# Kernel optimization log

Measured on AMD Instinct MI355X. Metric: run time of the kernel, lower is better.

The kernel has to match this reference:

```python
import jax, jax.numpy as jnp
import numpy as np

B, S, H = 2, 2048, 4096
NH, NKV, D = 32, 8, 128  # heads, kv heads, head_dim


def rotate_half(x):
    x1, x2 = jnp.split(x, 2, axis=-1)
    return jnp.concatenate((-x2, x1), axis=-1)


def setup_inputs() -> dict:
    key = jax.random.key(0)
    ks = jax.random.split(key, 5)
    hidden_states = jax.random.normal(ks[0], (B, S, H), jnp.float32) * 0.02
    wq = jax.random.normal(ks[1], (H, NH * D), jnp.float32) * 0.02
    wk = jax.random.normal(ks[2], (H, NKV * D), jnp.float32) * 0.02
    wv = jax.random.normal(ks[3], (H, NKV * D), jnp.float32) * 0.02
    wo = jax.random.normal(ks[4], (NH * D, H), jnp.float32) * 0.02
    # Llama rotary cache: emb = cat(freqs, freqs); cos/sin shape [S, D]
    inv_freq = 1.0 / (10000.0 ** (jnp.arange(0, D, 2, dtype=jnp.float32) / D))
    t = jnp.arange(S, dtype=jnp.float32)
    freqs = jnp.einsum('i,j->ij', t, inv_freq)
    emb = jnp.concatenate((freqs, freqs), axis=-1)
    cos, sin = jnp.cos(emb), jnp.sin(emb)
    # additive causal mask [S, S]
    causal = jnp.tril(jnp.ones((S, S), dtype=bool))
    attn_mask = jnp.where(causal, 0.0, -1e9).astype(jnp.float32)
    return {'hidden_states': hidden_states, 'wq': wq, 'wk': wk, 'wv': wv,
            'wo': wo, 'cos': cos, 'sin': sin, 'attn_mask': attn_mask}


def reference(hidden_states, wq, wk, wv, wo, cos, sin, attn_mask):
    b, s, _ = hidden_states.shape
    q = (hidden_states @ wq).reshape(b, s, NH, D)   # [b,s,nh,d]
    k = (hidden_states @ wk).reshape(b, s, NKV, D)  # [b,s,nkv,d]
    v = (hidden_states @ wv).reshape(b, s, NKV, D)
    c = cos[None, :, None, :]  # [1,s,1,d]
    sn = sin[None, :, None, :]
    q = q * c + rotate_half(q) * sn
    k = k * c + rotate_half(k) * sn
    # GQA: repeat KV heads to match query heads
    grp = NH // NKV
    k = jnp.repeat(k, grp, axis=2)
    v = jnp.repeat(v, grp, axis=2)
    scale = 1.0 / np.sqrt(D).astype(np.float32)
    scores = jnp.einsum('bqhd,bkhd->bhqk', q, k) * scale
    scores = scores + attn_mask[None, None, :, :]
    probs = jax.nn.softmax(scores, axis=-1)
    out = jnp.einsum('bhqk,bkhd->bqhd', probs, v).reshape(b, s, NH * D)
    return out @ wo
```

## Files before the change

### kernel.cpp

```cpp
#include <hip/hip_runtime.h>

typedef __attribute__((ext_vector_type(8))) short short8;
typedef __attribute__((ext_vector_type(4))) float f32x4;
typedef __attribute__((ext_vector_type(4))) int int4v;

__device__ __forceinline__ float bf2f(unsigned short u) {
  unsigned int x = ((unsigned int)u) << 16;
  float f;
  __builtin_memcpy(&f, &x, 4);
  return f;
}
__device__ __forceinline__ unsigned short f2bf(float f) {
  unsigned int x;
  __builtin_memcpy(&x, &f, 4);
  unsigned int r = (x + 0x7FFFu + ((x >> 16) & 1u)) >> 16;
  return (unsigned short)r;
}
__device__ __forceinline__ unsigned int cvtpk_bf16(float lo, float hi) {
  unsigned int r;
  asm("v_cvt_pk_bf16_f32 %0, %1, %2" : "=v"(r) : "v"(lo), "v"(hi));
  return r;
}
__device__ __forceinline__ float exp2_hw(float x) {
  float r;
  asm("v_exp_f32 %0, %1" : "=v"(r) : "v"(x));
  return r;
}
__device__ __forceinline__ int4v s8_to_i4(short8 v) {
  int4v r;
  __builtin_memcpy(&r, &v, 16);
  return r;
}
__device__ __forceinline__ short8 i4_to_s8(int4v v) {
  short8 r;
  __builtin_memcpy(&r, &v, 16);
  return r;
}
__device__ __forceinline__ short8 ld8_f32(const float* p) {
  f32x4 x = *(const f32x4*)p;
  f32x4 y = *(const f32x4*)(p + 4);
  short8 r;
  r[0] = (short)f2bf(x[0]); r[1] = (short)f2bf(x[1]);
  r[2] = (short)f2bf(x[2]); r[3] = (short)f2bf(x[3]);
  r[4] = (short)f2bf(y[0]); r[5] = (short)f2bf(y[1]);
  r[6] = (short)f2bf(y[2]); r[7] = (short)f2bf(y[3]);
  return r;
}

__device__ __forceinline__ void async16(unsigned short* lds, const unsigned short* g) {
  __builtin_amdgcn_global_load_lds(
      (const __attribute__((address_space(1))) void*)g,
      (__attribute__((address_space(3))) void*)lds, 16, 0, 0);
}

__global__ void downcast_f2b(const float* __restrict__ in,
                             unsigned short* __restrict__ out, int n8) {
  int i = blockIdx.x * 256 + threadIdx.x;
  if (i >= n8) return;
  *(short8*)(out + (size_t)i * 8) = ld8_f32(in + (size_t)i * 8);
}

__global__ void transpose64_f2b(const float* __restrict__ in,
                                unsigned short* __restrict__ out, int R, int C) {
  alignas(16) __shared__ unsigned short t[64][72];
  const int c0 = blockIdx.x * 64;
  const int r0 = blockIdx.y * 64;
  const int tid = threadIdx.x;
  const int rr = tid >> 4;
  const int cc = (tid & 15) << 2;
#pragma unroll
  for (int i = 0; i < 4; i++) {
    int r = rr + i * 16;
    f32x4 v = *(const f32x4*)(in + (size_t)(r0 + r) * C + c0 + cc);
#pragma unroll
    for (int j = 0; j < 4; j++) t[cc + j][r] = f2bf(v[j]);
  }
  __syncthreads();
  const int seg = tid & 7;
  const int cr = tid >> 3;
#pragma unroll
  for (int i = 0; i < 2; i++) {
    int c = cr + i * 32;
    short8 w = *(const short8*)&t[c][seg * 8];
    *(short8*)(out + (size_t)(c0 + c) * R + r0 + seg * 8) = w;
  }
}

#define MFMA16(AF, B0, B1, N0, N1)                                                   \
  _Pragma("unroll") for (int mi = 0; mi < 8; mi++) {                                 \
    acc[mi][N0] = __builtin_amdgcn_mfma_f32_16x16x32_bf16(AF[mi], B0, acc[mi][N0], 0, 0, 0); \
    acc[mi][N1] = __builtin_amdgcn_mfma_f32_16x16x32_bf16(AF[mi], B1, acc[mi][N1], 0, 0, 0); \
  }

#define STAGE8(BUF, SLOT, BASE, KOFF)                                     \
  do {                                                                    \
    async16(&lds[BUF][SLOT][tid * 8], (BASE) + (KOFF));                   \
    async16(&lds[BUF][SLOT][4096 + tid * 8], (BASE) + Kstep128 + (KOFF)); \
  } while (0)

#define BAR8 asm volatile("s_barrier" ::: "memory")

#define TILE8(CUR, UU, S0, S123, VM)                                                   \
  do {                                                                                 \
    const int kb = (UU)*64;                                                            \
    short8 af[8], b0, b1;                                                              \
                                                                       \
    _Pragma("unroll") for (int mi = 0; mi < 8; mi++)                                   \
        af[mi] = *(const short8*)(&lds[CUR][0][(wr * 128 + mi * 16 + fr) * 32 + fragoff]); \
    b0 = *(const short8*)(&lds[CUR][2][(wc * 64 + 0 * 16 + fr) * 32 + fragoff]);       \
    b1 = *(const short8*)(&lds[CUR][2][(wc * 64 + 1 * 16 + fr) * 32 + fragoff]);       \
    if (S0) STAGE8((CUR) ^ 1, 3, Bbase, kb + 96);                                      \
    BAR8;                                                                              \
    __builtin_amdgcn_s_setprio(1);                                                     \
    MFMA16(af, b0, b1, 0, 1);                                                          \
    __builtin_amdgcn_s_setprio(0);                                                     \
    BAR8;                                                                              \
                                                                       \
    b0 = *(const short8*)(&lds[CUR][2][(wc * 64 + 2 * 16 + fr) * 32 + fragoff]);       \
    b1 = *(const short8*)(&lds[CUR][2][(wc * 64 + 3 * 16 + fr) * 32 + fragoff]);       \
    if (S123) STAGE8(CUR, 0, Abase, kb + 128);                                         \
    BAR8;                                                                              \
    __builtin_amdgcn_s_setprio(1);                                                     \
    MFMA16(af, b0, b1, 2, 3);                                                          \
    __builtin_amdgcn_s_setprio(0);                                                     \
    BAR8;                                                                              \
                                                                       \
    _Pragma("unroll") for (int mi = 0; mi < 8; mi++)                                   \
        af[mi] = *(const short8*)(&lds[CUR][1][(wr * 128 + mi * 16 + fr) * 32 + fragoff]); \
    b0 = *(const short8*)(&lds[CUR][3][(wc * 64 + 0 * 16 + fr) * 32 + fragoff]);       \
    b1 = *(const short8*)(&lds[CUR][3][(wc * 64 + 1 * 16 + fr) * 32 + fragoff]);       \
    if (S123) STAGE8(CUR, 2, Bbase, kb + 128);                                         \
    BAR8;                                                                              \
    __builtin_amdgcn_s_setprio(1);                                                     \
    MFMA16(af, b0, b1, 0, 1);                                                          \
    __builtin_amdgcn_s_setprio(0);                                                     \
    BAR8;                                                                              \
                                                                       \
    b0 = *(const short8*)(&lds[CUR][3][(wc * 64 + 2 * 16 + fr) * 32 + fragoff]);       \
    b1 = *(const short8*)(&lds[CUR][3][(wc * 64 + 3 * 16 + fr) * 32 + fragoff]);       \
    if (S123) STAGE8(CUR, 1, Abase, kb + 160);                                         \
    BAR8;                                                                              \
    __builtin_amdgcn_s_setprio(1);                                                     \
    MFMA16(af, b0, b1, 2, 3);                                                          \
    __builtin_amdgcn_s_setprio(0);                                                     \
    if ((VM) == 6) {                                                                   \
      asm volatile("s_waitcnt vmcnt(6)" ::: "memory");                                 \
      __builtin_amdgcn_sched_barrier(0);                                               \
    } else if ((VM) == 0) {                                                            \
      asm volatile("s_waitcnt vmcnt(0)" ::: "memory");                                 \
      __builtin_amdgcn_sched_barrier(0);                                               \
    }                                                                                  \
    BAR8;                                                                              \
  } while (0)

template <int CF32>
__global__ __launch_bounds__(512, 2) void gemm8p(
    const unsigned short* __restrict__ A, const unsigned short* __restrict__ BT,
    void* __restrict__ Cp, int M, int N, int K) {
  alignas(16) __shared__ unsigned short lds[2][4][8192];
  const int tid = threadIdx.x;
  const int l = tid & 63;
  const int wv = tid >> 6;
  const int wr = wv >> 2, wc = wv & 3;

  const int nwg = gridDim.x * gridDim.y;
  int id = blockIdx.y * gridDim.x + blockIdx.x;
  id = (id & 7) * (nwg >> 3) + (id >> 3);
  const int bm = (id % gridDim.x) * 256;
  const int bn = (id / gridDim.x) * 256;

  const int fr = l & 15, hi = l >> 4;
  const int fragoff = ((hi ^ (((fr >> 3) & 1) << 1)) << 3);
  const int srow = tid >> 2;
  const int scol = (((tid & 3) ^ (((tid >> 5) & 1) << 1)) << 3);
  const unsigned short* Abase = A + (size_t)(bm + srow) * K + scol;
  const unsigned short* Bbase = BT + (size_t)(bn + srow) * K + scol;
  const size_t Kstep128 = (size_t)128 * K;

  f32x4 acc[8][4] = {};
  const int nt = K >> 6;

  STAGE8(0, 0, Abase, 0);
  STAGE8(0, 2, Bbase, 0);
  STAGE8(0, 1, Abase, 32);
  STAGE8(0, 3, Bbase, 32);
  STAGE8(1, 0, Abase, 64);
  STAGE8(1, 2, Bbase, 64);
  STAGE8(1, 1, Abase, 96);
  asm volatile("s_waitcnt vmcnt(6)" ::: "memory");
  __builtin_amdgcn_sched_barrier(0);
  BAR8;

  int U = 0;
  for (; U + 3 < nt; U += 2) {
    TILE8(0, U, 1, 1, 6);
    TILE8(1, U + 1, 1, 1, 6);
  }
  TILE8(0, nt - 2, 1, 0, 0);
  TILE8(1, nt - 1, 0, 0, -1);

  const int er = hi << 2;
#pragma unroll
  for (int mi = 0; mi < 8; mi++) {
#pragma unroll
    for (int ni = 0; ni < 4; ni++) {
      int row = bm + wr * 128 + mi * 16 + er;
      int col = bn + wc * 64 + ni * 16 + fr;
#pragma unroll
      for (int r = 0; r < 4; r++) {
        if constexpr (CF32)
          ((float*)Cp)[(size_t)(row + r) * N + col] = acc[mi][ni][r];
        else
          ((unsigned short*)Cp)[(size_t)(row + r) * N + col] = f2bf(acc[mi][ni][r]);
      }
    }
  }
}

__global__ void rope_qk(unsigned short* __restrict__ qkv,
                        const float* __restrict__ cosb,
                        const float* __restrict__ sinb, float qscale) {
  int gid = blockIdx.x * 256 + threadIdx.x;
  const int isK = gid >= 1048576;
  int g = isK ? gid - 1048576 : gid;
  const int nhs = isK ? 3 : 5;
  const int base = isK ? 4096 : 0;
  const float sc = isK ? 1.0f : qscale;
  int dblk = g & 7;
  int u2 = g >> 3;
  int head = u2 & ((1 << nhs) - 1);
  int token = u2 >> nhs;
  int s = token & 2047;
  int d0 = dblk << 3;
  unsigned short* p0 = qkv + (size_t)token * 6144 + base + (head << 7) + d0;
  unsigned short* p1 = p0 + 64;
  const float* cp = cosb + s * 128 + d0;
  const float* sp = sinb + s * 128 + d0;
  short8 a = *(const short8*)p0;
  short8 bq = *(const short8*)p1;
  f32x4 c0 = *(const f32x4*)cp, c1 = *(const f32x4*)(cp + 4);
  f32x4 s0 = *(const f32x4*)sp, s1 = *(const f32x4*)(sp + 4);
  short8 o0, o1;
#pragma unroll
  for (int j = 0; j < 8; j++) {
    float x0 = bf2f((unsigned short)a[j]);
    float x1 = bf2f((unsigned short)bq[j]);
    float c = (j < 4) ? c0[j & 3] : c1[j & 3];
    float sn = (j < 4) ? s0[j & 3] : s1[j & 3];
    o0[j] = (short)f2bf((x0 * c - x1 * sn) * sc);
    o1[j] = (short)f2bf((x1 * c + x0 * sn) * sc);
  }
  *(short8*)p0 = o0;
  *(short8*)p1 = o1;
}

#define NEGBIG -30000.0f

__device__ __forceinline__ int vswz(int d) { return (((d >> 3) ^ d) & 7) << 2; }

__device__ __forceinline__ void packV(const short8 vreg[4], int parity,
                                      unsigned int vw[4][4]) {
#pragma unroll
  for (int rep = 0; rep < 4; rep++) {
    int4v own = s8_to_i4(vreg[rep]);
    int4v oth;
#pragma unroll
    for (int q = 0; q < 4; q++) oth[q] = __shfl_xor(own[q], 16);
    unsigned int oA = parity ? (unsigned)own[2] : (unsigned)own[0];
    unsigned int oB = parity ? (unsigned)own[3] : (unsigned)own[1];
    unsigned int tA = parity ? (unsigned)oth[2] : (unsigned)oth[0];
    unsigned int tB = parity ? (unsigned)oth[3] : (unsigned)oth[1];
    unsigned int evA = parity ? tA : oA, odA = parity ? oA : tA;
    unsigned int evB = parity ? tB : oB, odB = parity ? oB : tB;
    vw[rep][0] = (evA & 0xFFFFu) | (odA << 16);
    vw[rep][1] = (evA >> 16) | (odA & 0xFFFF0000u);
    vw[rep][2] = (evB & 0xFFFFu) | (odB << 16);
    vw[rep][3] = (evB >> 16) | (odB & 0xFFFF0000u);
  }
}

__global__ __launch_bounds__(256, 2) void flash_attn(
    const unsigned short* __restrict__ QKV, unsigned short* __restrict__ O) {
  alignas(16) __shared__ unsigned short lK[2][64 * 128];
  alignas(16) __shared__ unsigned int lV[2][128 * 32];

  const int tid = threadIdx.x;
  const int lane = tid & 63;
  const int w = tid >> 6;
  const int b = blockIdx.z;
  const int h = blockIdx.y;
  const int xa = blockIdx.x;
  const int kvh = h >> 2;

  const int fr = lane & 15;
  const int hi = lane >> 4;
  const int fk8 = hi << 3;
  const int hi4 = hi << 2;

  const int srow = tid >> 4;
  const int sc8 = (tid & 15) << 3;
  const int parity = srow & 1;
  const int vd0 = sc8 + (parity << 2);
  const int kscol = sc8 ^ ((srow & 7) << 3);

  const unsigned short* Kbp = QKV + (size_t)(b * 2048) * 6144 + 4096 + kvh * 128;
  const unsigned short* Vbp = Kbp + 1024;

  short8 vreg[4];
  unsigned int vw[4][4];

#pragma unroll
  for (int rep = 0; rep < 4; rep++)
    async16(&lK[0][rep * 2048 + tid * 8],
            Kbp + (size_t)(rep * 16 + srow) * 6144 + kscol);
#pragma unroll
  for (int rep = 0; rep < 4; rep++)
    vreg[rep] = *(const short8*)(Vbp + (size_t)(rep * 16 + srow) * 6144 + sc8);
  packV(vreg, parity, vw);

  for (int pass = 0; pass < 2; pass++) {
    const int x = pass ? (15 - xa) : xa;
    const int q0 = x * 128;
    const int nt = 2 * x + 2;

    short8 qf[2][4];
#pragma unroll
    for (int qsub = 0; qsub < 2; qsub++) {
      const unsigned short* qb =
          QKV + (size_t)(b * 2048 + q0 + w * 32 + qsub * 16 + fr) * 6144 + h * 128 + fk8;
#pragma unroll
      for (int ks = 0; ks < 4; ks++) qf[qsub][ks] = *(const short8*)(qb + ks * 32);
    }

    f32x4 oacc[2][8] = {};
    float m2[2] = {NEGBIG, NEGBIG};
    float ls[2] = {0.f, 0.f};

    for (int t = 0; t < nt; t++) {
      const int c = t & 1;
#pragma unroll
      for (int rep = 0; rep < 4; rep++) {
        int kvp = rep * 8 + (srow >> 1);
#pragma unroll
        for (int j = 0; j < 4; j++)
          lV[c][(vd0 + j) * 32 + (kvp ^ vswz(vd0 + j))] = vw[rep][j];
      }
      __syncthreads();

      if (t + 1 < nt) {
        const int kv1 = (t + 1) * 64;
#pragma unroll
        for (int rep = 0; rep < 4; rep++)
          async16(&lK[c ^ 1][rep * 2048 + tid * 8],
                  Kbp + (size_t)(kv1 + rep * 16 + srow) * 6144 + kscol);
#pragma unroll
        for (int rep = 0; rep < 4; rep++)
          vreg[rep] = *(const short8*)(Vbp + (size_t)(kv1 + rep * 16 + srow) * 6144 + sc8);
      } else if (pass == 0) {
#pragma unroll
        for (int rep = 0; rep < 4; rep++)
          async16(&lK[c ^ 1][rep * 2048 + tid * 8],
                  Kbp + (size_t)(rep * 16 + srow) * 6144 + kscol);
#pragma unroll
        for (int rep = 0; rep < 4; rep++)
          vreg[rep] = *(const short8*)(Vbp + (size_t)(rep * 16 + srow) * 6144 + sc8);
      }

      f32x4 sacc[2][4] = {};
      __builtin_amdgcn_s_setprio(1);
#pragma unroll
      for (int fc = 0; fc < 4; fc++)
#pragma unroll
        for (int ks = 0; ks < 4; ks++) {
          short8 bk = *(const short8*)(&lK[c][(fc * 16 + fr) * 128 +
                                              ((ks * 32 + fk8) ^ ((fr & 7) << 3))]);
          sacc[0][fc] = __builtin_amdgcn_mfma_f32_16x16x32_bf16(bk, qf[0][ks], sacc[0][fc], 0, 0, 0);
          sacc[1][fc] = __builtin_amdgcn_mfma_f32_16x16x32_bf16(bk, qf[1][ks], sacc[1][fc], 0, 0, 0);
        }
      __builtin_amdgcn_s_setprio(0);

      const bool diag = (t >= nt - 2);
      const int kvb = t * 64;
      unsigned int pk[2][4][2];

#pragma unroll
      for (int qsub = 0; qsub < 2; qsub++) {
        const int q = q0 + w * 32 + qsub * 16 + fr;
        float sv[4][4];
#pragma unroll
        for (int fc = 0; fc < 4; fc++)
#pragma unroll
          for (int r = 0; r < 4; r++) {
            float xx = sacc[qsub][fc][r];
            if (diag && (kvb + fc * 16 + hi4 + r > q)) xx = NEGBIG;
            sv[fc][r] = xx;
          }
        float mx = sv[0][0];
#pragma unroll
        for (int fc = 0; fc < 4; fc++)
#pragma unroll
          for (int r = 0; r < 4; r++) mx = fmaxf(mx, sv[fc][r]);
        mx = fmaxf(mx, __shfl_xor(mx, 16));
        mx = fmaxf(mx, __shfl_xor(mx, 32));
        if (__any(mx > m2[qsub] + 8.0f)) {
          float mnew = fmaxf(m2[qsub], mx);
          float alpha = exp2_hw(m2[qsub] - mnew);
          m2[qsub] = mnew;
          ls[qsub] *= alpha;
          f32x4 av;
#pragma unroll
          for (int r = 0; r < 4; r++) av[r] = __shfl(alpha, hi4 + r);
#pragma unroll
          for (int nf = 0; nf < 8; nf++) oacc[qsub][nf] *= av;
        }
        float rs = 0.f;
        float p[4][4];
#pragma unroll
        for (int fc = 0; fc < 4; fc++)
#pragma unroll
          for (int r = 0; r < 4; r++) {
            p[fc][r] = exp2_hw(sv[fc][r] - m2[qsub]);
            rs += p[fc][r];
          }
        rs += __shfl_xor(rs, 16);
        rs += __shfl_xor(rs, 32);
        ls[qsub] += rs;
#pragma unroll
        for (int fc = 0; fc < 4; fc++) {
          pk[qsub][fc][0] = cvtpk_bf16(p[fc][0], p[fc][1]);
          pk[qsub][fc][1] = cvtpk_bf16(p[fc][2], p[fc][3]);
        }
      }

      const int src0 = fr + ((hi & 1) << 5);
      const int src1 = src0 + 16;
#pragma unroll
      for (int kvs = 0; kvs < 2; kvs++) {
        unsigned int aw[2][4];
#pragma unroll
        for (int qsub = 0; qsub < 2; qsub++) {
#pragma unroll
          for (int jj = 0; jj < 4; jj++) {
            int src = (jj < 2) ? src0 : src1;
            int rr = jj & 1;
            unsigned int y0 = (unsigned)__shfl((int)pk[qsub][kvs * 2][rr], src);
            unsigned int y1 = (unsigned)__shfl((int)pk[qsub][kvs * 2 + 1][rr], src);
            aw[qsub][jj] = (hi >> 1) ? y1 : y0;
          }
        }
        int4v a0i = {(int)aw[0][0], (int)aw[0][1], (int)aw[0][2], (int)aw[0][3]};
        int4v a1i = {(int)aw[1][0], (int)aw[1][1], (int)aw[1][2], (int)aw[1][3]};
        short8 af0 = i4_to_s8(a0i), af1 = i4_to_s8(a1i);
        __builtin_amdgcn_s_setprio(1);
#pragma unroll
        for (int nf = 0; nf < 8; nf++) {
          int row = nf * 16 + fr;
          int4v bvw = *(const int4v*)(&lV[c][row * 32 + ((kvs * 16 + hi4) ^ vswz(row))]);
          short8 bv = i4_to_s8(bvw);
          oacc[0][nf] = __builtin_amdgcn_mfma_f32_16x16x32_bf16(af0, bv, oacc[0][nf], 0, 0, 0);
          oacc[1][nf] = __builtin_amdgcn_mfma_f32_16x16x32_bf16(af1, bv, oacc[1][nf], 0, 0, 0);
        }
        __builtin_amdgcn_s_setprio(0);
      }

      packV(vreg, parity, vw);
    }

#pragma unroll
    for (int qsub = 0; qsub < 2; qsub++) {
      f32x4 iv;
#pragma unroll
      for (int r = 0; r < 4; r++) iv[r] = 1.0f / __shfl(ls[qsub], hi4 + r);
#pragma unroll
      for (int r = 0; r < 4; r++) {
        unsigned short* op =
            O + (size_t)(b * 2048 + q0 + w * 32 + qsub * 16 + hi4 + r) * 4096 + h * 128 + fr;
#pragma unroll
        for (int nf = 0; nf < 8; nf++) op[nf * 16] = f2bf(oacc[qsub][nf][r] * iv[r]);
      }
    }
  }
}

extern "C" void kernel_launch(void* const* d_in, const int* in_sizes, int n_in,
                              void* d_out, int out_size, void* d_ws, size_t ws_size,
                              hipStream_t stream) {
  const float* hs = (const float*)d_in[0];
  const float* wq = (const float*)d_in[1];
  const float* wk = (const float*)d_in[2];
  const float* wv = (const float*)d_in[3];
  const float* wo = (const float*)d_in[4];
  const float* cosb = (const float*)d_in[5];
  const float* sinb = (const float*)d_in[6];

  unsigned short* ws = (unsigned short*)d_ws;
  unsigned short* T1 = ws;
  unsigned short* T2 = T1 + 16777216;
  unsigned short* T3 = T2 + 4194304;
  unsigned short* QKV = T3 + 4194304;
  unsigned short* Ob = QKV + 25165824;

  unsigned short* hsb = (unsigned short*)d_out;

  downcast_f2b<<<8192, 256, 0, stream>>>(hs, hsb, 2097152);
  transpose64_f2b<<<dim3(64, 64), 256, 0, stream>>>(wq, T1, 4096, 4096);
  transpose64_f2b<<<dim3(16, 64), 256, 0, stream>>>(wk, T2, 4096, 1024);
  transpose64_f2b<<<dim3(16, 64), 256, 0, stream>>>(wv, T3, 4096, 1024);

  gemm8p<0><<<dim3(16, 24), 512, 0, stream>>>(hsb, T1, QKV, 4096, 6144, 4096);

  transpose64_f2b<<<dim3(64, 64), 256, 0, stream>>>(wo, T1, 4096, 4096);

  const float qscale = 0.08838834764831845f * 1.4426950408889634f;
  rope_qk<<<5120, 256, 0, stream>>>(QKV, cosb, sinb, qscale);

  flash_attn<<<dim3(8, 32, 2), 256, 0, stream>>>(QKV, Ob);

  gemm8p<1><<<dim3(16, 16), 512, 0, stream>>>(Ob, T1, (float*)d_out, 4096, 4096, 4096);
}
```

Measured before the change: 528.3 us.

## Add smaller-tile double-buffered GEMM for QKV projection with XCD-aware block remap

Measured after the change: 536.5 us. Within noise of the previous version (+1.5%).

```diff
diff --git a/kernel.cpp b/kernel.cpp
--- a/kernel.cpp
+++ b/kernel.cpp
@@ -215,6 +215,86 @@
       }
     }
   }
+}
+
+__global__ __launch_bounds__(512, 4) void gemm2(
+    const unsigned short* __restrict__ A, const unsigned short* __restrict__ BT,
+    unsigned short* __restrict__ Cp, int M, int N, int K) {
+  alignas(16) __shared__ unsigned short lds[2][12288];
+  const int tid = threadIdx.x;
+  const int l = tid & 63;
+  const int wv = tid >> 6;
+  const int wr = wv >> 2;
+  const int wc = wv & 3;
+
+  const int nwg = gridDim.x * gridDim.y;
+  int id = blockIdx.y * gridDim.x + blockIdx.x;
+  id = (id & 7) * (nwg >> 3) + (id >> 3);
+  const int bm = (id % gridDim.x) * 256;
+  const int bn = (id / gridDim.x) * 128;
+
+  const int fr = l & 15, hi = l >> 4;
+  const int fragoff = ((hi ^ (((fr >> 3) & 1) << 1)) << 3);
+  const int srow = tid >> 2;
+  const int scol = (((tid & 3) ^ (((tid >> 5) & 1) << 1)) << 3);
+  const unsigned short* Abase = A + (size_t)(bm + srow) * K + scol;
+  const unsigned short* Bbase = BT + (size_t)(bn + srow) * K + scol;
+  const size_t Kstep128 = (size_t)128 * K;
+
+  f32x4 acc[8][2] = {};
+  const int nt = K >> 5;
+
+#define G2_STAGE(BUF, KOFF)                                              \
+  do {                                                                   \
+    async16(&lds[BUF][tid * 8], Abase + (KOFF));                         \
+    async16(&lds[BUF][4096 + tid * 8], Abase + Kstep128 + (KOFF));       \
+    async16(&lds[BUF][8192 + tid * 8], Bbase + (KOFF));                  \
+  } while (0)
+
+  G2_STAGE(0, 0);
+  G2_STAGE(1, 32);
+  asm volatile("s_waitcnt vmcnt(3)" ::: "memory");
+  __builtin_amdgcn_sched_barrier(0);
+  BAR8;
+
+  for (int t = 0; t < nt; ++t) {
+    const int cur = t & 1;
+    short8 a[8], b0, b1;
+#pragma unroll
+    for (int mi = 0; mi < 8; mi++)
+      a[mi] = *(const short8*)(&lds[cur][(wr * 128 + mi * 16 + fr) * 32 + fragoff]);
+    b0 = *(const short8*)(&lds[cur][8192 + (wc * 32 + fr) * 32 + fragoff]);
+    b1 = *(const short8*)(&lds[cur][8192 + (wc * 32 + 16 + fr) * 32 + fragoff]);
+    BAR8;
+    if (t + 2 < nt) G2_STAGE(cur, (t + 2) * 32);
+    __builtin_amdgcn_s_setprio(1);
+#pragma unroll
+    for (int mi = 0; mi < 8; mi++) {
+      acc[mi][0] = __builtin_amdgcn_mfma_f32_16x16x32_bf16(a[mi], b0, acc[mi][0], 0, 0, 0);
+      acc[mi][1] = __builtin_amdgcn_mfma_f32_16x16x32_bf16(a[mi], b1, acc[mi][1], 0, 0, 0);
+    }
+    __builtin_amdgcn_s_setprio(0);
+    if (t + 2 < nt)
+      asm volatile("s_waitcnt vmcnt(3)" ::: "memory");
+    else
+      asm volatile("s_waitcnt vmcnt(0)" ::: "memory");
+    __builtin_amdgcn_sched_barrier(0);
+    BAR8;
+  }
+
+  const int er = hi << 2;
+#pragma unroll
+  for (int mi = 0; mi < 8; mi++) {
+#pragma unroll
+    for (int ni = 0; ni < 2; ni++) {
+      int row = bm + wr * 128 + mi * 16 + er;
+      int col = bn + wc * 32 + ni * 16 + fr;
+#pragma unroll
+      for (int r = 0; r < 4; r++)
+        Cp[(size_t)(row + r) * N + col] = f2bf(acc[mi][ni][r]);
+    }
+  }
+#undef G2_STAGE
 }
 
 __global__ void rope_qk(unsigned short* __restrict__ qkv,
@@ -507,7 +587,7 @@
   transpose64_f2b<<<dim3(16, 64), 256, 0, stream>>>(wk, T2, 4096, 1024);
   transpose64_f2b<<<dim3(16, 64), 256, 0, stream>>>(wv, T3, 4096, 1024);
 
-  gemm8p<0><<<dim3(16, 24), 512, 0, stream>>>(hsb, T1, QKV, 4096, 6144, 4096);
+  gemm2<<<dim3(16, 48), 512, 0, stream>>>(hsb, T1, QKV, 4096, 6144, 4096);
 
   transpose64_f2b<<<dim3(64, 64), 256, 0, stream>>>(wo, T1, 4096, 4096);
 
```
